# Optimization experiments

Hardware: AMD Instinct MI355X
Metric: run time of the kernel (lower is better)

Reference implementation:

```python
import jax, jax.numpy as jnp
import numpy as np

N = 50000
E = 800000
NEG_SLOPE = 0.2


def gatv2_layer(x, src, dst, Wl, Wr, att, bias, heads, ch):
    # x: [N, Fin]; Wl/Wr: [Fin, heads*ch]; att: [heads, ch]; bias: [heads*ch]
    xl = (x @ Wl).reshape(N, heads, ch)  # source transform
    xr = (x @ Wr).reshape(N, heads, ch)  # target transform
    e = xl[src] + xr[dst]                              # [E, H, C]
    s = jnp.einsum('ehc,hc->eh', jax.nn.leaky_relu(e, NEG_SLOPE), att)  # [E, H]
    # scatter-softmax over incoming edges of each target node
    smax = jax.ops.segment_max(s, dst, num_segments=N)  # [N, H]
    ex = jnp.exp(s - smax[dst])
    denom = jax.ops.segment_sum(ex, dst, num_segments=N)
    alpha = ex / denom[dst]                             # [E, H]
    out = jax.ops.segment_sum(xl[src] * alpha[..., None], dst, num_segments=N)  # [N, H, C]
    return out.reshape(N, heads * ch) + bias


def setup_inputs() -> dict:
    key = jax.random.key(0)
    ks = jax.random.split(key, 12)
    x = jax.random.normal(ks[0], (N, 128), dtype=jnp.float32)
    edge_index = jax.random.randint(ks[1], (2, E), 0, N, dtype=jnp.int64)
    edge_attr = jax.random.normal(ks[2], (E, 16), dtype=jnp.float32)
    s1 = 1.0 / np.sqrt(128.0)
    # layer 1: 128 -> 64, heads=2 (concat -> 128)
    Wl1 = jax.random.normal(ks[3], (128, 128), dtype=jnp.float32) * s1
    Wr1 = jax.random.normal(ks[4], (128, 128), dtype=jnp.float32) * s1
    att1 = jax.random.normal(ks[5], (2, 64), dtype=jnp.float32) * 0.1
    b1 = jnp.zeros((128,), dtype=jnp.float32)
    # layer 2: 128 -> 128, heads=1
    Wl2 = jax.random.normal(ks[6], (128, 128), dtype=jnp.float32) * s1
    Wr2 = jax.random.normal(ks[7], (128, 128), dtype=jnp.float32) * s1
    att2 = jax.random.normal(ks[8], (1, 128), dtype=jnp.float32) * 0.1
    b2 = jnp.zeros((128,), dtype=jnp.float32)
    return {"x": x, "edge_index": edge_index, "edge_attr": edge_attr,
            "Wl1": Wl1, "Wr1": Wr1, "att1": att1, "b1": b1,
            "Wl2": Wl2, "Wr2": Wr2, "att2": att2, "b2": b2}


def reference(x, edge_index, edge_attr, Wl1, Wr1, att1, b1, Wl2, Wr2, att2, b2):
    # using_edge_attr=False default path: edge_attr ignored.
    # GATv2Conv default add_self_loops=True
    loops = jnp.arange(N, dtype=edge_index.dtype)
    src = jnp.concatenate([edge_index[0], loops])
    dst = jnp.concatenate([edge_index[1], loops])
    h = gatv2_layer(x, src, dst, Wl1, Wr1, att1, b1, heads=2, ch=64)
    out = gatv2_layer(h, src, dst, Wl2, Wr2, att2, b2, heads=1, ch=128)
    return out
```

## Files before the change

### kernel.cpp

```cpp
#include <hip/hip_runtime.h>

#define NEG_SLOPE 0.2f
#define NPB 256
#define CHUNK 4096

typedef _Float16 f16x8 __attribute__((ext_vector_type(8)));
typedef _Float16 f16x4 __attribute__((ext_vector_type(4)));
typedef _Float16 f16x2 __attribute__((ext_vector_type(2)));
typedef float    f32x4 __attribute__((ext_vector_type(4)));

#if defined(__has_builtin)
#if __has_builtin(__builtin_amdgcn_fdot2)
#define HAVE_FDOT2 1
#endif
#endif

__device__ __forceinline__ f32x4 cvt4(f16x4 v) {
    return __builtin_convertvector(v, f32x4);
}

__global__ __launch_bounds__(256) void prep_kernel(
    const float* __restrict__ W0, const float* __restrict__ W1,
    const float* __restrict__ W2, const float* __restrict__ W3,
    _Float16* __restrict__ wt,
    const float* __restrict__ x, _Float16* __restrict__ xh,
    _Float16* __restrict__ xlo, int total, int* __restrict__ bcnt)
{
    int t = threadIdx.x;
    if (blockIdx.x < 256) {
        if (blockIdx.x == 0) bcnt[t] = 0;
        int idx = blockIdx.x * 256 + t;
        int m = idx >> 14;
        int k = (idx >> 7) & 127;
        int n = idx & 127;
        const float* W = (m == 0) ? W0 : (m == 1) ? W1 : (m == 2) ? W2 : W3;
        wt[m * 16384 + n * 128 + k] = (_Float16)W[k * 128 + n];
    } else {
        int i = (blockIdx.x - 256) * 256 + t;
        if (i * 2 < total) {
            float2 f = *(const float2*)(x + (size_t)i * 2);
            _Float16 h0 = (_Float16)f.x, h1 = (_Float16)f.y;
            _Float16 l0 = (_Float16)(f.x - (float)h0), l1 = (_Float16)(f.y - (float)h1);
            *(f16x2*)(xh  + (size_t)i * 2) = (f16x2){h0, h1};
            *(f16x2*)(xlo + (size_t)i * 2) = (f16x2){l0, l1};
        }
    }
}

__global__ __launch_bounds__(256) void gemm_f16_kernel(
    const _Float16* __restrict__ Ahi, const _Float16* __restrict__ Alo,
    const _Float16* __restrict__ Wt0, const _Float16* __restrict__ Wt1,
    _Float16* __restrict__ Cl, _Float16* __restrict__ Cr, int N)
{
    const _Float16* Wt = blockIdx.y ? Wt1 : Wt0;
    _Float16* C = blockIdx.y ? Cr : Cl;

    __shared__ _Float16 ldsW[128 * 136];

    const int tid = threadIdx.x;
    const int wave = tid >> 6;
    const int lane = tid & 63;
    const int mrow = lane & 15;
    const int quad = lane >> 4;
    const int rbase = blockIdx.x * 128 + wave * 32;

    const int sn = tid >> 1, shf = tid & 1;
    float4 stg[8];
    {
        const float4* g = (const float4*)(Wt + sn * 128 + shf * 64);
#pragma unroll
        for (int j = 0; j < 8; j++) stg[j] = g[j];
    }

    f16x8 ah[2][4], al[2][4];
#pragma unroll
    for (int rt = 0; rt < 2; rt++) {
        int r = rbase + rt * 16 + mrow;
        if (r > N - 1) r = N - 1;
        const _Float16* pa = Ahi + (size_t)r * 128 + quad * 8;
        const _Float16* pl = Alo + (size_t)r * 128 + quad * 8;
#pragma unroll
        for (int s = 0; s < 4; s++) {
            ah[rt][s] = *(const f16x8*)(pa + s * 32);
            al[rt][s] = *(const f16x8*)(pl + s * 32);
        }
    }

    {
        float4* d = (float4*)&ldsW[sn * 136 + shf * 64];
#pragma unroll
        for (int j = 0; j < 8; j++) d[j] = stg[j];
    }

    f32x4 acc[2][8];
#pragma unroll
    for (int rt = 0; rt < 2; rt++)
#pragma unroll
        for (int c = 0; c < 8; c++) acc[rt][c] = (f32x4){0.f, 0.f, 0.f, 0.f};

    __syncthreads();

#pragma unroll
    for (int s = 0; s < 4; s++) {
#pragma unroll
        for (int c = 0; c < 8; c++) {
            f16x8 bw = *(const f16x8*)&ldsW[(c * 16 + mrow) * 136 + s * 32 + quad * 8];
            acc[0][c] = __builtin_amdgcn_mfma_f32_16x16x32_f16(ah[0][s], bw, acc[0][c], 0, 0, 0);
            acc[0][c] = __builtin_amdgcn_mfma_f32_16x16x32_f16(al[0][s], bw, acc[0][c], 0, 0, 0);
            acc[1][c] = __builtin_amdgcn_mfma_f32_16x16x32_f16(ah[1][s], bw, acc[1][c], 0, 0, 0);
            acc[1][c] = __builtin_amdgcn_mfma_f32_16x16x32_f16(al[1][s], bw, acc[1][c], 0, 0, 0);
        }
    }

#pragma unroll
    for (int rt = 0; rt < 2; rt++)
#pragma unroll
        for (int i = 0; i < 4; i++) {
            int r = rbase + rt * 16 + quad * 4 + i;
            if (r < N) {
                _Float16* cr = C + (size_t)r * 128 + mrow;
#pragma unroll
                for (int c = 0; c < 8; c++) cr[c * 16] = (_Float16)acc[rt][c][i];
            }
        }
}

__global__ __launch_bounds__(256) void histB_kernel(
    const int* __restrict__ ei, int* __restrict__ bcnt, int E)
{
    __shared__ int bh[256];
    int t = threadIdx.x;
    bh[t] = 0;
    __syncthreads();
    int base = blockIdx.x * CHUNK;
#pragma unroll
    for (int j = 0; j < CHUNK / 256; j++) {
        int e = base + t + j * 256;
        if (e < E) atomicAdd(&bh[ei[E + e] >> 8], 1);
    }
    __syncthreads();
    if (bh[t]) atomicAdd(&bcnt[t], bh[t]);
}

__global__ __launch_bounds__(256) void scanB_kernel(
    const int* __restrict__ bcnt, int* __restrict__ bstart,
    int* __restrict__ gcursor, int NB, int E)
{
    __shared__ int s[256];
    int t = threadIdx.x;
    int v = (t < NB) ? bcnt[t] : 0;
    s[t] = v;
    __syncthreads();
    for (int off = 1; off < 256; off <<= 1) {
        int u = (t >= off) ? s[t - off] : 0;
        __syncthreads();
        s[t] += u;
        __syncthreads();
    }
    if (t < NB) { bstart[t] = s[t] - v; gcursor[t] = s[t] - v; }
    if (t == 0) bstart[NB] = E;
}

__global__ __launch_bounds__(256) void passA_kernel(
    const int* __restrict__ ei, int* __restrict__ gcursor,
    int2* __restrict__ staging, int E)
{
    __shared__ int bh[256];
    __shared__ int bbase[256];
    int t = threadIdx.x;
    bh[t] = 0;
    __syncthreads();
    int base = blockIdx.x * CHUNK;
    int srcv[16], dstv[16], rb[16];
#pragma unroll
    for (int j = 0; j < 16; j++) {
        int e = base + t + j * 256;
        if (e < E) {
            int d = ei[E + e];
            srcv[j] = ei[e];
            dstv[j] = d;
            int bk = d >> 8;
            int r = atomicAdd(&bh[bk], 1);
            rb[j] = (r << 8) | bk;
        } else rb[j] = -1;
    }
    __syncthreads();
    if (bh[t]) bbase[t] = atomicAdd(&gcursor[t], bh[t]);
    __syncthreads();
#pragma unroll
    for (int j = 0; j < 16; j++) {
        if (rb[j] >= 0) {
            int bk = rb[j] & 255, r = rb[j] >> 8;
            staging[bbase[bk] + r] = make_int2(srcv[j], dstv[j]);
        }
    }
}

__global__ __launch_bounds__(256) void passB_kernel(
    const int2* __restrict__ staging, const int* __restrict__ bstart,
    int* __restrict__ start, int* __restrict__ sorted_src, int N, int E)
{
    __shared__ int lhist[256], lscan[256], lcur[256];
    int b = blockIdx.x, t = threadIdx.x;
    int r0 = bstart[b], r1 = bstart[b + 1];
    lhist[t] = 0;
    __syncthreads();
    for (int i = r0 + t; i < r1; i += 256) atomicAdd(&lhist[staging[i].y & 255], 1);
    __syncthreads();
    int v = lhist[t];
    lscan[t] = v;
    __syncthreads();
    for (int off = 1; off < 256; off <<= 1) {
        int u = (t >= off) ? lscan[t - off] : 0;
        __syncthreads();
        lscan[t] += u;
        __syncthreads();
    }
    int excl = lscan[t] - v;
    int node = b * NPB + t;
    if (node < N) start[node] = r0 + excl;
    lcur[t] = excl;
    if (b == 0 && t == 0) start[N] = E;
    __syncthreads();
    for (int i = r0 + t; i < r1; i += 256) {
        int2 p = staging[i];
        int rank = atomicAdd(&lcur[p.y & 255], 1);
        sorted_src[r0 + rank] = p.x;
    }
}

template <int H, bool BFOUT>
__global__ __launch_bounds__(256) void gat_fused_kernel(
    const _Float16* __restrict__ xl, const _Float16* __restrict__ xr,
    const float* __restrict__ att, const float* __restrict__ bias,
    const int* __restrict__ start, const int* __restrict__ sorted_src,
    float* __restrict__ outf, _Float16* __restrict__ oh,
    _Float16* __restrict__ ol, int N)
{
    int node = blockIdx.x * 4 + (threadIdx.x >> 6);
    if (node >= N) return;
    const int lane = threadIdx.x & 63;
    const int half = lane >> 5;
    const int hl   = lane & 31;
    const int RED  = (H == 2) ? 8 : 16;
    const _Float16 NS = (_Float16)NEG_SLOPE;

    const f16x4 b4 = *(const f16x4*)(xr + (size_t)node * 128 + hl * 4);
    float4 attf = *(const float4*)(att + hl * 4);
    const float L2E = 1.44269504f;
    f16x4 av = {(_Float16)(attf.x * L2E), (_Float16)(attf.y * L2E),
                (_Float16)(attf.z * L2E), (_Float16)(attf.w * L2E)};
#if defined(HAVE_FDOT2)
    f16x2 avlo = __builtin_shufflevector(av, av, 0, 1);
    f16x2 avhi = __builtin_shufflevector(av, av, 2, 3);
#else
    f32x4 avf = cvt4(av);
#endif

#define SCORE(a_, p_) {                                                     \
        f16x4 t_ = (a_) + b4;                                               \
        f16x4 u_ = __builtin_elementwise_max(t_, t_ * NS);                  \
        _Float16 dummy_;                                                    \
        (void)dummy_;                                                       \
                                                \
        p_ = 0.f;                                                           \
        score_dot(u_, p_);                                                  \
    }

    auto score_dot = [&](f16x4 u_, float& p_) {
#if defined(HAVE_FDOT2)
        f16x2 ulo = __builtin_shufflevector(u_, u_, 0, 1);
        f16x2 uhi = __builtin_shufflevector(u_, u_, 2, 3);
        p_ = __builtin_amdgcn_fdot2(ulo, avlo,
             __builtin_amdgcn_fdot2(uhi, avhi, 0.0f, false), false);
#else
        f32x4 uf = cvt4(u_);
        p_ = uf[0] * avf[0] + uf[1] * avf[1] + uf[2] * avf[2] + uf[3] * avf[3];
#endif
    };

    f32x4 acc = (f32x4){0.f, 0.f, 0.f, 0.f};
    float den = 0.f;

    const int s0 = start[node];
    const int s1 = start[node + 1];
    const int M  = s1 - s0 + 1;
    const int Ksafe = (M - 1) >> 1;
    const int K     = (M + 1) >> 1;

    int k = 0;
    for (; k + 8 <= Ksafe; k += 8) {
        int src[8]; f16x4 a[8]; float p[8];
#pragma unroll
        for (int j = 0; j < 8; j++) {
            int iv = 2 * (k + j) + half;
            src[j] = (iv == 0) ? node : sorted_src[s0 + iv - 1];
        }
#pragma unroll
        for (int j = 0; j < 8; j++)
            a[j] = *(const f16x4*)(xl + (size_t)src[j] * 128 + hl * 4);
#pragma unroll
        for (int j = 0; j < 8; j++) SCORE(a[j], p[j]);
#pragma unroll
        for (int m = 1; m <= RED; m <<= 1) {
#pragma unroll
            for (int j = 0; j < 8; j++) p[j] += __shfl_xor(p[j], m, 64);
        }
#pragma unroll
        for (int j = 0; j < 8; j++) {
            float e = exp2f(p[j]);
            den += e;
            acc = acc + cvt4(a[j]) * e;
        }
    }
    for (; k + 4 <= Ksafe; k += 4) {
        int src[4]; f16x4 a[4]; float p[4];
#pragma unroll
        for (int j = 0; j < 4; j++) {
            int iv = 2 * (k + j) + half;
            src[j] = (iv == 0) ? node : sorted_src[s0 + iv - 1];
        }
#pragma unroll
        for (int j = 0; j < 4; j++)
            a[j] = *(const f16x4*)(xl + (size_t)src[j] * 128 + hl * 4);
#pragma unroll
        for (int j = 0; j < 4; j++) SCORE(a[j], p[j]);
#pragma unroll
        for (int m = 1; m <= RED; m <<= 1) {
#pragma unroll
            for (int j = 0; j < 4; j++) p[j] += __shfl_xor(p[j], m, 64);
        }
#pragma unroll
        for (int j = 0; j < 4; j++) {
            float e = exp2f(p[j]);
            den += e;
            acc = acc + cvt4(a[j]) * e;
        }
    }
    for (; k < Ksafe; k++) {
        int iv = 2 * k + half;
        int src = (iv == 0) ? node : sorted_src[s0 + iv - 1];
        f16x4 a = *(const f16x4*)(xl + (size_t)src * 128 + hl * 4);
        float p; SCORE(a, p);
#pragma unroll
        for (int m = 1; m <= RED; m <<= 1) p += __shfl_xor(p, m, 64);
        float e = exp2f(p);
        den += e;
        acc = acc + cvt4(a) * e;
    }
    for (; k < K; k++) {
        int iv = 2 * k + half;
        bool valid = iv < M;
        int pos = s0 + (iv > 0 ? iv - 1 : 0);
        int ld = sorted_src[pos];
        int src = (iv == 0) ? node : (valid ? ld : node);
        f16x4 a = *(const f16x4*)(xl + (size_t)src * 128 + hl * 4);
        float p; SCORE(a, p);
#pragma unroll
        for (int m = 1; m <= RED; m <<= 1) p += __shfl_xor(p, m, 64);
        float e = valid ? exp2f(p) : 0.f;
        den += e;
        acc = acc + cvt4(a) * e;
    }
#undef SCORE

    den    += __shfl_xor(den,    32, 64);
    acc[0] += __shfl_xor(acc[0], 32, 64);
    acc[1] += __shfl_xor(acc[1], 32, 64);
    acc[2] += __shfl_xor(acc[2], 32, 64);
    acc[3] += __shfl_xor(acc[3], 32, 64);

    float inv = 1.0f / den;
    float4 bi = *(const float4*)(bias + hl * 4);
    float o0 = acc[0] * inv + bi.x;
    float o1 = acc[1] * inv + bi.y;
    float o2 = acc[2] * inv + bi.z;
    float o3 = acc[3] * inv + bi.w;

    if (lane < 32) {
        if (BFOUT) {
            _Float16 h0 = (_Float16)o0, h1 = (_Float16)o1, h2 = (_Float16)o2, h3 = (_Float16)o3;
            f16x4 hv = {h0, h1, h2, h3};
            f16x4 lv = {(_Float16)(o0 - (float)h0), (_Float16)(o1 - (float)h1),
                        (_Float16)(o2 - (float)h2), (_Float16)(o3 - (float)h3)};
            *(f16x4*)(oh + (size_t)node * 128 + hl * 4) = hv;
            *(f16x4*)(ol + (size_t)node * 128 + hl * 4) = lv;
        } else {
            *(float4*)(outf + (size_t)node * 128 + hl * 4) = make_float4(o0, o1, o2, o3);
        }
    }
}

extern "C" void kernel_launch(void* const* d_in, const int* in_sizes, int n_in,
                              void* d_out, int out_size, void* d_ws, size_t ws_size,
                              hipStream_t stream)
{
    const float* x    = (const float*)d_in[0];
    const int*   ei   = (const int*)d_in[1];
    const float* Wl1  = (const float*)d_in[3];
    const float* Wr1  = (const float*)d_in[4];
    const float* att1 = (const float*)d_in[5];
    const float* b1   = (const float*)d_in[6];
    const float* Wl2  = (const float*)d_in[7];
    const float* Wr2  = (const float*)d_in[8];
    const float* att2 = (const float*)d_in[9];
    const float* b2   = (const float*)d_in[10];
    float* out = (float*)d_out;

    const int N  = in_sizes[0] / 128;
    const int E  = in_sizes[1] / 2;
    const int NB = (N + NPB - 1) / NPB;

    const size_t nf = (size_t)N * 128;
    _Float16* xlf  = (_Float16*)d_ws;
    _Float16* xrf  = xlf + nf;
    _Float16* ah   = xrf + nf;
    _Float16* al   = ah + nf;
    _Float16* wt   = al + nf;
    int* bcnt      = (int*)(wt + 4 * 16384);
    int* bstart    = bcnt + 256;
    int* gcursor   = bstart + 257;
    int* start     = gcursor + 256;
    size_t stgoff  = ((size_t)(start + N + 1) + 7) & ~(size_t)7;
    int2* staging  = (int2*)stgoff;
    int* sorted_src = (int*)(staging + E);

    const int grid_chunk = (E + CHUNK - 1) / CHUNK;
    const int node_grid  = (N + 3) / 4;
    const int gemm_gx    = (N + 127) / 128;
    const int split_grid = (int)((nf / 2 + 255) / 256);

    prep_kernel<<<256 + split_grid, 256, 0, stream>>>(
        Wl1, Wr1, Wl2, Wr2, wt, x, ah, al, (int)nf, bcnt);

    histB_kernel<<<grid_chunk, 256, 0, stream>>>(ei, bcnt, E);
    scanB_kernel<<<1, 256, 0, stream>>>(bcnt, bstart, gcursor, NB, E);
    passA_kernel<<<grid_chunk, 256, 0, stream>>>(ei, gcursor, staging, E);
    passB_kernel<<<NB, 256, 0, stream>>>(staging, bstart, start, sorted_src, N, E);

    gemm_f16_kernel<<<dim3(gemm_gx, 2), 256, 0, stream>>>(
        ah, al, wt + 0 * 16384, wt + 1 * 16384, xlf, xrf, N);
    gat_fused_kernel<2, true><<<node_grid, 256, 0, stream>>>(
        xlf, xrf, att1, b1, start, sorted_src, nullptr, ah, al, N);

    gemm_f16_kernel<<<dim3(gemm_gx, 2), 256, 0, stream>>>(
        ah, al, wt + 2 * 16384, wt + 3 * 16384, xlf, xrf, N);
    gat_fused_kernel<1, false><<<node_grid, 256, 0, stream>>>(
        xlf, xrf, att2, b2, start, sorted_src, out, nullptr, nullptr, N);
}
```

Measured before the change: 304.3 us.

## Process four edges per wavefront with 16-byte loads and DPP reductions

Restructures the fused GAT aggregation kernel so each 64-lane wavefront handles four edges at once, with 16 lanes per edge each loading 8 halfs (16-byte loads) instead of 32 lanes loading 4 halfs. The per-edge score reduction now uses DPP row operations instead of cross-lane shuffles, and the unrolled batches shrink to 4/2/1. This aims to raise memory-level parallelism on the gathers and cut shuffle cost, at the price of more accumulator registers and a wider final cross-group reduction.

```diff
diff --git a/kernel.cpp b/kernel.cpp
--- a/kernel.cpp
+++ b/kernel.cpp
@@ -8,6 +8,7 @@
 typedef _Float16 f16x4 __attribute__((ext_vector_type(4)));
 typedef _Float16 f16x2 __attribute__((ext_vector_type(2)));
 typedef float    f32x4 __attribute__((ext_vector_type(4)));
+typedef float    f32x8 __attribute__((ext_vector_type(8)));
 
 #if defined(__has_builtin)
 #if __has_builtin(__builtin_amdgcn_fdot2)
@@ -15,8 +16,15 @@
 #endif
 #endif
 
-__device__ __forceinline__ f32x4 cvt4(f16x4 v) {
-    return __builtin_convertvector(v, f32x4);
+__device__ __forceinline__ f32x8 cvt8(f16x8 v) {
+    return __builtin_convertvector(v, f32x8);
+}
+
+template <int CTRL>
+__device__ __forceinline__ float dpp_add(float v) {
+    int o = __builtin_amdgcn_update_dpp(0, __builtin_bit_cast(int, v),
+                                        CTRL, 0xF, 0xF, true);
+    return v + __builtin_bit_cast(float, o);
 }
 
 __global__ __launch_bounds__(256) void prep_kernel(
@@ -240,153 +248,135 @@
     int node = blockIdx.x * 4 + (threadIdx.x >> 6);
     if (node >= N) return;
     const int lane = threadIdx.x & 63;
-    const int half = lane >> 5;
-    const int hl   = lane & 31;
-    const int RED  = (H == 2) ? 8 : 16;
+    const int g  = lane >> 4;
+    const int hl = lane & 15;
     const _Float16 NS = (_Float16)NEG_SLOPE;
-
-    const f16x4 b4 = *(const f16x4*)(xr + (size_t)node * 128 + hl * 4);
-    float4 attf = *(const float4*)(att + hl * 4);
     const float L2E = 1.44269504f;
-    f16x4 av = {(_Float16)(attf.x * L2E), (_Float16)(attf.y * L2E),
-                (_Float16)(attf.z * L2E), (_Float16)(attf.w * L2E)};
+
+    const f16x8 b4 = *(const f16x8*)(xr + (size_t)node * 128 + hl * 8);
+    float4 at0 = *(const float4*)(att + hl * 8);
+    float4 at1 = *(const float4*)(att + hl * 8 + 4);
 #if defined(HAVE_FDOT2)
-    f16x2 avlo = __builtin_shufflevector(av, av, 0, 1);
-    f16x2 avhi = __builtin_shufflevector(av, av, 2, 3);
+    f16x2 av0 = {(_Float16)(at0.x * L2E), (_Float16)(at0.y * L2E)};
+    f16x2 av1 = {(_Float16)(at0.z * L2E), (_Float16)(at0.w * L2E)};
+    f16x2 av2 = {(_Float16)(at1.x * L2E), (_Float16)(at1.y * L2E)};
+    f16x2 av3 = {(_Float16)(at1.z * L2E), (_Float16)(at1.w * L2E)};
 #else
-    f32x4 avf = cvt4(av);
+    f32x8 avf = {at0.x * L2E, at0.y * L2E, at0.z * L2E, at0.w * L2E,
+                 at1.x * L2E, at1.y * L2E, at1.z * L2E, at1.w * L2E};
 #endif
 
-#define SCORE(a_, p_) {                                                     \
-        f16x4 t_ = (a_) + b4;                                               \
-        f16x4 u_ = __builtin_elementwise_max(t_, t_ * NS);                  \
-        _Float16 dummy_;                                                    \
-        (void)dummy_;                                                       \
-                                                \
-        p_ = 0.f;                                                           \
-        score_dot(u_, p_);                                                  \
-    }
-
-    auto score_dot = [&](f16x4 u_, float& p_) {
+    auto score = [&](f16x8 a_) -> float {
+        f16x8 t = a_ + b4;
+        f16x8 u = __builtin_elementwise_max(t, t * NS);
 #if defined(HAVE_FDOT2)
-        f16x2 ulo = __builtin_shufflevector(u_, u_, 0, 1);
-        f16x2 uhi = __builtin_shufflevector(u_, u_, 2, 3);
-        p_ = __builtin_amdgcn_fdot2(ulo, avlo,
-             __builtin_amdgcn_fdot2(uhi, avhi, 0.0f, false), false);
+        f16x2 u0 = __builtin_shufflevector(u, u, 0, 1);
+        f16x2 u1 = __builtin_shufflevector(u, u, 2, 3);
+        f16x2 u2 = __builtin_shufflevector(u, u, 4, 5);
+        f16x2 u3 = __builtin_shufflevector(u, u, 6, 7);
+        return __builtin_amdgcn_fdot2(u0, av0,
+               __builtin_amdgcn_fdot2(u1, av1,
+               __builtin_amdgcn_fdot2(u2, av2,
+               __builtin_amdgcn_fdot2(u3, av3, 0.f, false), false), false), false);
 #else
-        f32x4 uf = cvt4(u_);
-        p_ = uf[0] * avf[0] + uf[1] * avf[1] + uf[2] * avf[2] + uf[3] * avf[3];
+        f32x8 uf = cvt8(u);
+        float p = 0.f;
+#pragma unroll
+        for (int i = 0; i < 8; i++) p += uf[i] * avf[i];
+        return p;
 #endif
     };
 
-    f32x4 acc = (f32x4){0.f, 0.f, 0.f, 0.f};
+    auto red = [&](float p) -> float {
+        p = dpp_add<0xB1>(p);
+        p = dpp_add<0x4E>(p);
+        p = dpp_add<0x141>(p);
+        if (H == 1) p = dpp_add<0x140>(p);
+        return p;
+    };
+
+    f32x8 acc = {0.f, 0.f, 0.f, 0.f, 0.f, 0.f, 0.f, 0.f};
     float den = 0.f;
 
     const int s0 = start[node];
     const int s1 = start[node + 1];
     const int M  = s1 - s0 + 1;
-    const int Ksafe = (M - 1) >> 1;
-    const int K     = (M + 1) >> 1;
+    const int Kfull = M >> 2;
+    const int K     = (M + 3) >> 2;
+
+#define GBODY(B) {                                                          \
+        int srcv[B]; f16x8 a[B]; float p[B];                                \
+        _Pragma("unroll")                                                   \
+        for (int j = 0; j < B; j++) {                                       \
+            int iv = 4 * (k + j) + g;                                       \
+            int ld = sorted_src[s0 + ((iv > 0) ? iv - 1 : 0)];              \
+            srcv[j] = (iv == 0) ? node : ld;                                \
+        }                                                                   \
+        _Pragma("unroll")                                                   \
+        for (int j = 0; j < B; j++)                                         \
+            a[j] = *(const f16x8*)(xl + (size_t)srcv[j] * 128 + hl * 8);    \
+        _Pragma("unroll")                                                   \
+        for (int j = 0; j < B; j++) p[j] = score(a[j]);                     \
+        _Pragma("unroll")                                                   \
+        for (int j = 0; j < B; j++) p[j] = red(p[j]);                       \
+        _Pragma("unroll")                                                   \
+        for (int j = 0; j < B; j++) {                                       \
+            float e = exp2f(p[j]);                                          \
+            den += e;                                                       \
+            acc = acc + cvt8(a[j]) * e;                                     \
+        }                                                                   \
+    }
 
     int k = 0;
-    for (; k + 8 <= Ksafe; k += 8) {
-        int src[8]; f16x4 a[8]; float p[8];
-#pragma unroll
-        for (int j = 0; j < 8; j++) {
-            int iv = 2 * (k + j) + half;
-            src[j] = (iv == 0) ? node : sorted_src[s0 + iv - 1];
-        }
-#pragma unroll
-        for (int j = 0; j < 8; j++)
-            a[j] = *(const f16x4*)(xl + (size_t)src[j] * 128 + hl * 4);
-#pragma unroll
-        for (int j = 0; j < 8; j++) SCORE(a[j], p[j]);
-#pragma unroll
-        for (int m = 1; m <= RED; m <<= 1) {
-#pragma unroll
-            for (int j = 0; j < 8; j++) p[j] += __shfl_xor(p[j], m, 64);
-        }
-#pragma unroll
-        for (int j = 0; j < 8; j++) {
-            float e = exp2f(p[j]);
-            den += e;
-            acc = acc + cvt4(a[j]) * e;
-        }
-    }
-    for (; k + 4 <= Ksafe; k += 4) {
-        int src[4]; f16x4 a[4]; float p[4];
-#pragma unroll
-        for (int j = 0; j < 4; j++) {
-            int iv = 2 * (k + j) + half;
-            src[j] = (iv == 0) ? node : sorted_src[s0 + iv - 1];
-        }
-#pragma unroll
-        for (int j = 0; j < 4; j++)
-            a[j] = *(const f16x4*)(xl + (size_t)src[j] * 128 + hl * 4);
-#pragma unroll
-        for (int j = 0; j < 4; j++) SCORE(a[j], p[j]);
-#pragma unroll
-        for (int m = 1; m <= RED; m <<= 1) {
-#pragma unroll
-            for (int j = 0; j < 4; j++) p[j] += __shfl_xor(p[j], m, 64);
-        }
-#pragma unroll
-        for (int j = 0; j < 4; j++) {
-            float e = exp2f(p[j]);
-            den += e;
-            acc = acc + cvt4(a[j]) * e;
-        }
-    }
-    for (; k < Ksafe; k++) {
-        int iv = 2 * k + half;
-        int src = (iv == 0) ? node : sorted_src[s0 + iv - 1];
-        f16x4 a = *(const f16x4*)(xl + (size_t)src * 128 + hl * 4);
-        float p; SCORE(a, p);
-#pragma unroll
-        for (int m = 1; m <= RED; m <<= 1) p += __shfl_xor(p, m, 64);
-        float e = exp2f(p);
-        den += e;
-        acc = acc + cvt4(a) * e;
-    }
-    for (; k < K; k++) {
-        int iv = 2 * k + half;
+    for (; k + 4 <= Kfull; k += 4) GBODY(4)
+    if (k + 2 <= Kfull) { GBODY(2) k += 2; }
+    if (k < Kfull)      { GBODY(1) k += 1; }
+    if (k < K) {
+        int iv = 4 * k + g;
         bool valid = iv < M;
-        int pos = s0 + (iv > 0 ? iv - 1 : 0);
-        int ld = sorted_src[pos];
+        int ld = sorted_src[s0 + ((iv > 0) ? iv - 1 : 0)];
         int src = (iv == 0) ? node : (valid ? ld : node);
-        f16x4 a = *(const f16x4*)(xl + (size_t)src * 128 + hl * 4);
-        float p; SCORE(a, p);
-#pragma unroll
-        for (int m = 1; m <= RED; m <<= 1) p += __shfl_xor(p, m, 64);
+        f16x8 a = *(const f16x8*)(xl + (size_t)src * 128 + hl * 8);
+        float p = red(score(a));
         float e = valid ? exp2f(p) : 0.f;
         den += e;
-        acc = acc + cvt4(a) * e;
-    }
-#undef SCORE
-
-    den    += __shfl_xor(den,    32, 64);
-    acc[0] += __shfl_xor(acc[0], 32, 64);
-    acc[1] += __shfl_xor(acc[1], 32, 64);
-    acc[2] += __shfl_xor(acc[2], 32, 64);
-    acc[3] += __shfl_xor(acc[3], 32, 64);
+        acc = acc + cvt8(a) * e;
+    }
+#undef GBODY
+
+    den += __shfl_xor(den, 16, 64);
+    den += __shfl_xor(den, 32, 64);
+#pragma unroll
+    for (int i = 0; i < 8; i++) {
+        acc[i] += __shfl_xor(acc[i], 16, 64);
+        acc[i] += __shfl_xor(acc[i], 32, 64);
+    }
 
     float inv = 1.0f / den;
-    float4 bi = *(const float4*)(bias + hl * 4);
-    float o0 = acc[0] * inv + bi.x;
-    float o1 = acc[1] * inv + bi.y;
-    float o2 = acc[2] * inv + bi.z;
-    float o3 = acc[3] * inv + bi.w;
-
-    if (lane < 32) {
+    float4 bi0 = *(const float4*)(bias + hl * 8);
+    float4 bi1 = *(const float4*)(bias + hl * 8 + 4);
+    float o[8];
+    o[0] = acc[0] * inv + bi0.x;  o[1] = acc[1] * inv + bi0.y;
+    o[2] = acc[2] * inv + bi0.z;  o[3] = acc[3] * inv + bi0.w;
+    o[4] = acc[4] * inv + bi1.x;  o[5] = acc[5] * inv + bi1.y;
+    o[6] = acc[6] * inv + bi1.z;  o[7] = acc[7] * inv + bi1.w;
+
+    if (lane < 16) {
         if (BFOUT) {
-            _Float16 h0 = (_Float16)o0, h1 = (_Float16)o1, h2 = (_Float16)o2, h3 = (_Float16)o3;
-            f16x4 hv = {h0, h1, h2, h3};
-            f16x4 lv = {(_Float16)(o0 - (float)h0), (_Float16)(o1 - (float)h1),
-                        (_Float16)(o2 - (float)h2), (_Float16)(o3 - (float)h3)};
-            *(f16x4*)(oh + (size_t)node * 128 + hl * 4) = hv;
-            *(f16x4*)(ol + (size_t)node * 128 + hl * 4) = lv;
+            f16x8 hv, lv;
+#pragma unroll
+            for (int i = 0; i < 8; i++) {
+                _Float16 h = (_Float16)o[i];
+                hv[i] = h;
+                lv[i] = (_Float16)(o[i] - (float)h);
+            }
+            *(f16x8*)(oh + (size_t)node * 128 + hl * 8) = hv;
+            *(f16x8*)(ol + (size_t)node * 128 + hl * 8) = lv;
         } else {
-            *(float4*)(outf + (size_t)node * 128 + hl * 4) = make_float4(o0, o1, o2, o3);
+            *(float4*)(outf + (size_t)node * 128 + hl * 8) =
+                make_float4(o[0], o[1], o[2], o[3]);
+            *(float4*)(outf + (size_t)node * 128 + hl * 8 + 4) =
+                make_float4(o[4], o[5], o[6], o[7]);
         }
     }
 }
```

Measured after the change: 300.9 us. About the same (-1.1%).
